# Optimization experiments

Measured on AMD Instinct MI355X. Metric: run time of the kernel, lower is better.

## Reference

```python
import jax, jax.numpy as jnp
import numpy as np

L = 8192
E = 1024
H = 16
D = E // H  # head_dim = 64


def setup_inputs() -> dict:
    key = jax.random.key(0)
    ks = jax.random.split(key, 5)
    x = jax.random.normal(ks[0], (L, E), dtype=jnp.float32)
    in_proj_weight = jax.random.normal(ks[1], (3 * E, E), dtype=jnp.float32) * (1.0 / np.sqrt(E))
    in_proj_bias = jax.random.normal(ks[2], (3 * E,), dtype=jnp.float32) * 0.02
    out_proj_weight = jax.random.normal(ks[3], (E, E), dtype=jnp.float32) * (1.0 / np.sqrt(E))
    out_proj_bias = jax.random.normal(ks[4], (E,), dtype=jnp.float32) * 0.02
    return {
        "x": x,
        "in_proj_weight": in_proj_weight,
        "in_proj_bias": in_proj_bias,
        "out_proj_weight": out_proj_weight,
        "out_proj_bias": out_proj_bias,
    }


def reference(x, in_proj_weight, in_proj_bias, out_proj_weight, out_proj_bias):
    # Single-token query (decode-style): q from x[:1], k/v from full sequence.
    q = x[:1] @ in_proj_weight[:E].T + in_proj_bias[:E]            # [1, E]
    k = x @ in_proj_weight[E:2 * E].T + in_proj_bias[E:2 * E]      # [L, E]
    v = x @ in_proj_weight[2 * E:].T + in_proj_bias[2 * E:]        # [L, E]

    q = q.reshape(1, H, D).transpose(1, 0, 2)   # [H, 1, D]
    k = k.reshape(L, H, D).transpose(1, 2, 0)   # [H, D, L]
    v = v.reshape(L, H, D).transpose(1, 0, 2)   # [H, L, D]

    scale = 1.0 / np.sqrt(D).astype(np.float32)
    dot = jnp.matmul(q, k) * scale              # [H, 1, L]
    attn = jax.nn.softmax(dot, axis=-1)
    out = jnp.matmul(attn, v)                   # [H, 1, D]
    out = out.transpose(1, 0, 2).reshape(1, E)  # [1, E]
    return out @ out_proj_weight.T + out_proj_bias
```

## Files before the change

kernel.cpp:

```cpp
#include <hip/hip_runtime.h>

#define LSEQ 8192
#define E 1024
#define H 16
#define NSHARD 16

typedef __attribute__((ext_vector_type(8))) short short8;
typedef __attribute__((ext_vector_type(4))) float f32x4;

__device__ inline float bf2f(unsigned int u16) {
    union { unsigned int i; float f; } v;
    v.i = (u16 & 0xffffu) << 16;
    return v.f;
}

__device__ inline unsigned short f2bf(float f) {
    union { float f; unsigned int i; } v; v.f = f;
    unsigned int x = v.i;
    return (unsigned short)((x + 0x7fffu + ((x >> 16) & 1u)) >> 16);
}

__device__ inline float wave_reduce_sum(float v) {
    #pragma unroll
    for (int off = 32; off > 0; off >>= 1) v += __shfl_xor(v, off, 64);
    return v;
}

__global__ __launch_bounds__(256) void k0_q(
    const float* __restrict__ x, const float* __restrict__ W,
    const float* __restrict__ bias, float* __restrict__ q_ws,
    float* __restrict__ S_shard)
{
    if (blockIdx.x == 0) S_shard[threadIdx.x] = 0.f;
    int wave = threadIdx.x >> 6, lane = threadIdx.x & 63;
    int i = blockIdx.x * 4 + wave;
    const f32x4* wp = (const f32x4*)(W + i * E) + lane * 4;
    const f32x4* xp = (const f32x4*)(x) + lane * 4;
    float s = 0.f;
    #pragma unroll
    for (int j = 0; j < 4; j++) {
        f32x4 w4 = wp[j], x4 = xp[j];
        s += w4[0]*x4[0] + w4[1]*x4[1] + w4[2]*x4[2] + w4[3]*x4[3];
    }
    s = wave_reduce_sum(s);
    if (lane == 0) q_ws[i] = s + bias[i];
}

__global__ __launch_bounds__(256) void k1_rc(
    const float* __restrict__ W, const float* __restrict__ bias,
    const float* __restrict__ q_ws, unsigned short* __restrict__ r_bf,
    float* __restrict__ c_ws)
{
    __shared__ float red[4][64];
    int hb = blockIdx.x >> 4, ec = blockIdx.x & 15;
    int lane = threadIdx.x & 63, wq = threadIdx.x >> 6;
    int e = ec * 64 + lane;
    const float* qh = q_ws + hb * 64;
    float acc = 0.f;
    #pragma unroll
    for (int i = 0; i < 16; i++) {
        int d = wq * 16 + i;
        acc += qh[d] * W[(E + hb * 64 + d) * E + e];
    }
    red[wq][lane] = acc;
    __syncthreads();
    if (wq == 0) {
        float s = red[0][lane] + red[1][lane] + red[2][lane] + red[3][lane];
        r_bf[hb * E + e] = f2bf(s * 0.125f);
    }
    if (ec == 0 && wq == 1) {
        float v = qh[lane] * bias[E + hb * 64 + lane];
        v = wave_reduce_sum(v);
        if (lane == 0) c_ws[hb] = v * 0.125f;
    }
}

__global__ __launch_bounds__(512, 1) void k2_fused(
    const float* __restrict__ x,
    const unsigned short* __restrict__ r_bf,
    const float* __restrict__ c_ws,
    unsigned int* __restrict__ partial_bf, float* __restrict__ S_shard)
{
    __shared__ float x_lds[16 * 1028];
    __shared__ float sp[8 * 64 * 4];
    __shared__ float p_lds[16 * 16];
    __shared__ float esum[16];

    const int tid  = threadIdx.x;
    const int wave = tid >> 6, lane = tid & 63;
    const int beta = blockIdx.x;

    if (tid < 16) esum[tid] = 0.f;
    float acc[32];
    #pragma unroll
    for (int i = 0; i < 32; i++) acc[i] = 0.f;
    int lbase = beta * 32;

    for (int t = 0; t < 2; t++) {
        int R0 = lbase + t * 16;
        __syncthreads();
        {
            int row = tid >> 5, ch = tid & 31;
            const f32x4* src = (const f32x4*)(x + (R0 + row) * E);
            float* dst = x_lds + row * 1028;
            #pragma unroll
            for (int j = 0; j < 8; j++) {
                int c4 = ch + 32 * j;
                *(f32x4*)(dst + c4 * 4) = src[c4];
            }
        }
        __syncthreads();
        {
            int rw = lane & 15, quad = lane >> 4;
            f32x4 sacc = {0.f, 0.f, 0.f, 0.f};
            const float* arow = x_lds + rw * 1028 + wave * 128 + quad * 8;
            const short8* bp = (const short8*)(r_bf + rw * E + wave * 128 + quad * 8);
            #pragma unroll
            for (int kk = 0; kk < 4; kk++) {
                f32x4 a0 = *(const f32x4*)(arow + kk * 32);
                f32x4 a1 = *(const f32x4*)(arow + kk * 32 + 4);
                short8 af;
                af[0] = (short)f2bf(a0[0]); af[1] = (short)f2bf(a0[1]);
                af[2] = (short)f2bf(a0[2]); af[3] = (short)f2bf(a0[3]);
                af[4] = (short)f2bf(a1[0]); af[5] = (short)f2bf(a1[1]);
                af[6] = (short)f2bf(a1[2]); af[7] = (short)f2bf(a1[3]);
                short8 bfr = bp[kk * 4];
                sacc = __builtin_amdgcn_mfma_f32_16x16x32_bf16(af, bfr, sacc, 0, 0, 0);
            }
            *(f32x4*)&sp[(wave * 64 + lane) * 4] = sacc;
        }
        __syncthreads();
        if (tid < 256) {
            int m = tid >> 4, hh = tid & 15;
            int ln = (m >> 2) * 16 + hh, rg = m & 3;
            float s = c_ws[hh];
            #pragma unroll
            for (int w = 0; w < 8; w++) s += sp[(w * 64 + ln) * 4 + rg];
            float p = __expf(s);
            p_lds[m * 16 + hh] = p;
            atomicAdd(&esum[hh], p);
        }
        __syncthreads();
        #pragma unroll 4
        for (int m = 0; m < 16; m++) {
            float2 xv = *(const float2*)&x_lds[m * 1028 + tid * 2];
            const f32x4* pp = (const f32x4*)&p_lds[m * 16];
            #pragma unroll
            for (int g = 0; g < 4; g++) {
                f32x4 pv = pp[g];
                acc[(g * 4 + 0) * 2 + 0] += pv[0] * xv.x;
                acc[(g * 4 + 0) * 2 + 1] += pv[0] * xv.y;
                acc[(g * 4 + 1) * 2 + 0] += pv[1] * xv.x;
                acc[(g * 4 + 1) * 2 + 1] += pv[1] * xv.y;
                acc[(g * 4 + 2) * 2 + 0] += pv[2] * xv.x;
                acc[(g * 4 + 2) * 2 + 1] += pv[2] * xv.y;
                acc[(g * 4 + 3) * 2 + 0] += pv[3] * xv.x;
                acc[(g * 4 + 3) * 2 + 1] += pv[3] * xv.y;
            }
        }
    }
    __syncthreads();
    #pragma unroll
    for (int h = 0; h < 16; h++) {
        unsigned int pk = (unsigned int)f2bf(acc[h * 2])
                        | ((unsigned int)f2bf(acc[h * 2 + 1]) << 16);
        partial_bf[(beta * 16 + h) * 512 + tid] = pk;
    }
    if (tid < 16) atomicAdd(&S_shard[(beta & 15) * 16 + tid], esum[tid]);
}

__global__ __launch_bounds__(512) void k3_reduce(
    const unsigned int* __restrict__ partial_bf, float2* __restrict__ u_ws2)
{
    __shared__ float red[8][64][2];
    int wave = threadIdx.x >> 6, lane = threadIdx.x & 63;
    int col = blockIdx.x * 64 + lane;
    float s0 = 0.f, s1 = 0.f;
    #pragma unroll 8
    for (int bb = wave; bb < 256; bb += 8) {
        unsigned int v = partial_bf[bb * 8192 + col];
        s0 += bf2f(v);
        s1 += bf2f(v >> 16);
    }
    red[wave][lane][0] = s0;
    red[wave][lane][1] = s1;
    __syncthreads();
    if (wave == 0) {
        float t0 = 0.f, t1 = 0.f;
        #pragma unroll
        for (int w = 0; w < 8; w++) { t0 += red[w][lane][0]; t1 += red[w][lane][1]; }
        float2 o; o.x = t0; o.y = t1;
        u_ws2[col] = o;
    }
}

__global__ __launch_bounds__(256) void k4_oh(
    const float* __restrict__ W, const float* __restrict__ bias,
    const float* __restrict__ u_ws, const float* __restrict__ S_shard,
    float* __restrict__ oh_ws)
{
    int wave = threadIdx.x >> 6, lane = threadIdx.x & 63;
    int i = blockIdx.x * 4 + wave;
    int h = i >> 6;
    float Sh = 0.f;
    #pragma unroll
    for (int sh = 0; sh < NSHARD; sh++) Sh += S_shard[sh * 16 + h];
    const f32x4* wp = (const f32x4*)(W + (2 * E + i) * E) + lane * 4;
    const f32x4* up = (const f32x4*)(u_ws + h * E) + lane * 4;
    float s = 0.f;
    #pragma unroll
    for (int j = 0; j < 4; j++) {
        f32x4 w4 = wp[j], u4 = up[j];
        s += w4[0]*u4[0] + w4[1]*u4[1] + w4[2]*u4[2] + w4[3]*u4[3];
    }
    s = wave_reduce_sum(s);
    if (lane == 0) oh_ws[i] = s / Sh + bias[2 * E + i];
}

__global__ __launch_bounds__(256) void k5_out(
    const float* __restrict__ Wout, const float* __restrict__ bout,
    const float* __restrict__ oh_ws, float* __restrict__ out)
{
    int wave = threadIdx.x >> 6, lane = threadIdx.x & 63;
    int j = blockIdx.x * 4 + wave;
    const f32x4* wp = (const f32x4*)(Wout + j * E) + lane * 4;
    const f32x4* op = (const f32x4*)(oh_ws) + lane * 4;
    float s = 0.f;
    #pragma unroll
    for (int jj = 0; jj < 4; jj++) {
        f32x4 w4 = wp[jj], o4 = op[jj];
        s += w4[0]*o4[0] + w4[1]*o4[1] + w4[2]*o4[2] + w4[3]*o4[3];
    }
    s = wave_reduce_sum(s);
    if (lane == 0) out[j] = s + bout[j];
}

extern "C" void kernel_launch(void* const* d_in, const int* in_sizes, int n_in,
                              void* d_out, int out_size, void* d_ws, size_t ws_size,
                              hipStream_t stream) {
    const float* x  = (const float*)d_in[0];
    const float* W  = (const float*)d_in[1];
    const float* b  = (const float*)d_in[2];
    const float* Wo = (const float*)d_in[3];
    const float* bo = (const float*)d_in[4];
    float* out = (float*)d_out;
    char* ws = (char*)d_ws;

    float* c_ws    = (float*)(ws);
    float* S_shard = (float*)(ws + 1024);
    float* oh_ws   = (float*)(ws + 4096);
    float* q_ws    = (float*)(ws + 12288);
    unsigned short* r_bf = (unsigned short*)(ws + 16384);
    float* u_ws    = (float*)(ws + 65536);
    unsigned int* partial_bf = (unsigned int*)(ws + 131072);

    hipLaunchKernelGGL(k0_q,     dim3(256), dim3(256), 0, stream,
                       x, W, b, q_ws, S_shard);
    hipLaunchKernelGGL(k1_rc,    dim3(256), dim3(256), 0, stream,
                       W, b, q_ws, r_bf, c_ws);
    hipLaunchKernelGGL(k2_fused, dim3(256), dim3(512), 0, stream,
                       x, r_bf, c_ws, partial_bf, S_shard);
    hipLaunchKernelGGL(k3_reduce, dim3(128), dim3(512), 0, stream,
                       partial_bf, (float2*)u_ws);
    hipLaunchKernelGGL(k4_oh,    dim3(256), dim3(256), 0, stream,
                       W, b, u_ws, S_shard, oh_ws);
    hipLaunchKernelGGL(k5_out,   dim3(256), dim3(256), 0, stream,
                       Wo, bo, oh_ws, out);
}
```

Before: 108.8 us.

## Halve k2 grid with 1024-thread blocks and register-prefetch next x tile

The fused score/accumulate kernel now runs 128 blocks of 1024 threads, each covering 64 sequence rows in four 16-row tiles instead of 256 blocks of 512 threads over 32 rows. The next tile of x is prefetched into registers while the current one is processed, to overlap global loads with compute. Each thread now owns one column instead of two and packs bf16 pairs via a lane shuffle. The reduction kernel reads half as many partials. The risk is that only 128 blocks leave half the CUs idle on a 256-CU part, and that per-block serial work goes up.

```diff
diff --git a/kernel.cpp b/kernel.cpp
--- a/kernel.cpp
+++ b/kernel.cpp
@@ -4,6 +4,7 @@
 #define E 1024
 #define H 16
 #define NSHARD 16
+#define NCHUNK 128
 
 typedef __attribute__((ext_vector_type(8))) short short8;
 typedef __attribute__((ext_vector_type(4))) float f32x4;
@@ -75,48 +76,56 @@
     }
 }
 
-__global__ __launch_bounds__(512, 1) void k2_fused(
+__global__ __launch_bounds__(1024, 1) void k2_fused(
     const float* __restrict__ x,
     const unsigned short* __restrict__ r_bf,
     const float* __restrict__ c_ws,
     unsigned int* __restrict__ partial_bf, float* __restrict__ S_shard)
 {
     __shared__ float x_lds[16 * 1028];
-    __shared__ float sp[8 * 64 * 4];
+    __shared__ float sp[16 * 64 * 4];
     __shared__ float p_lds[16 * 16];
     __shared__ float esum[16];
 
     const int tid  = threadIdx.x;
     const int wave = tid >> 6, lane = tid & 63;
     const int beta = blockIdx.x;
+    const int lbase = beta * 64;
 
     if (tid < 16) esum[tid] = 0.f;
-    float acc[32];
-    #pragma unroll
-    for (int i = 0; i < 32; i++) acc[i] = 0.f;
-    int lbase = beta * 32;
-
-    for (int t = 0; t < 2; t++) {
-        int R0 = lbase + t * 16;
+    float acc[16];
+    #pragma unroll
+    for (int i = 0; i < 16; i++) acc[i] = 0.f;
+
+    const int srow = tid >> 6, sch = tid & 63;
+    f32x4 pre[4];
+    {
+        const f32x4* src = (const f32x4*)(x + (lbase + srow) * E);
+        #pragma unroll
+        for (int j = 0; j < 4; j++) pre[j] = src[sch + 64 * j];
+    }
+
+    for (int t = 0; t < 4; t++) {
         __syncthreads();
         {
-            int row = tid >> 5, ch = tid & 31;
-            const f32x4* src = (const f32x4*)(x + (R0 + row) * E);
-            float* dst = x_lds + row * 1028;
-            #pragma unroll
-            for (int j = 0; j < 8; j++) {
-                int c4 = ch + 32 * j;
-                *(f32x4*)(dst + c4 * 4) = src[c4];
-            }
+            float* dst = x_lds + srow * 1028;
+            #pragma unroll
+            for (int j = 0; j < 4; j++) *(f32x4*)(dst + (sch + 64 * j) * 4) = pre[j];
+        }
+        {
+            int nt = (t + 1) & 3;
+            const f32x4* src = (const f32x4*)(x + (lbase + nt * 16 + srow) * E);
+            #pragma unroll
+            for (int j = 0; j < 4; j++) pre[j] = src[sch + 64 * j];
         }
         __syncthreads();
         {
             int rw = lane & 15, quad = lane >> 4;
             f32x4 sacc = {0.f, 0.f, 0.f, 0.f};
-            const float* arow = x_lds + rw * 1028 + wave * 128 + quad * 8;
-            const short8* bp = (const short8*)(r_bf + rw * E + wave * 128 + quad * 8);
-            #pragma unroll
-            for (int kk = 0; kk < 4; kk++) {
+            const float* arow = x_lds + rw * 1028 + wave * 64 + quad * 8;
+            const short8* bp = (const short8*)(r_bf + rw * E + wave * 64 + quad * 8);
+            #pragma unroll
+            for (int kk = 0; kk < 2; kk++) {
                 f32x4 a0 = *(const f32x4*)(arow + kk * 32);
                 f32x4 a1 = *(const f32x4*)(arow + kk * 32 + 4);
                 short8 af;
@@ -135,7 +144,7 @@
             int ln = (m >> 2) * 16 + hh, rg = m & 3;
             float s = c_ws[hh];
             #pragma unroll
-            for (int w = 0; w < 8; w++) s += sp[(w * 64 + ln) * 4 + rg];
+            for (int w = 0; w < 16; w++) s += sp[(w * 64 + ln) * 4 + rg];
             float p = __expf(s);
             p_lds[m * 16 + hh] = p;
             atomicAdd(&esum[hh], p);
@@ -143,30 +152,29 @@
         __syncthreads();
         #pragma unroll 4
         for (int m = 0; m < 16; m++) {
-            float2 xv = *(const float2*)&x_lds[m * 1028 + tid * 2];
+            float xv = x_lds[m * 1028 + tid];
             const f32x4* pp = (const f32x4*)&p_lds[m * 16];
             #pragma unroll
             for (int g = 0; g < 4; g++) {
                 f32x4 pv = pp[g];
-                acc[(g * 4 + 0) * 2 + 0] += pv[0] * xv.x;
-                acc[(g * 4 + 0) * 2 + 1] += pv[0] * xv.y;
-                acc[(g * 4 + 1) * 2 + 0] += pv[1] * xv.x;
-                acc[(g * 4 + 1) * 2 + 1] += pv[1] * xv.y;
-                acc[(g * 4 + 2) * 2 + 0] += pv[2] * xv.x;
-                acc[(g * 4 + 2) * 2 + 1] += pv[2] * xv.y;
-                acc[(g * 4 + 3) * 2 + 0] += pv[3] * xv.x;
-                acc[(g * 4 + 3) * 2 + 1] += pv[3] * xv.y;
+                acc[g * 4 + 0] += pv[0] * xv;
+                acc[g * 4 + 1] += pv[1] * xv;
+                acc[g * 4 + 2] += pv[2] * xv;
+                acc[g * 4 + 3] += pv[3] * xv;
             }
         }
     }
     __syncthreads();
-    #pragma unroll
-    for (int h = 0; h < 16; h++) {
-        unsigned int pk = (unsigned int)f2bf(acc[h * 2])
-                        | ((unsigned int)f2bf(acc[h * 2 + 1]) << 16);
-        partial_bf[(beta * 16 + h) * 512 + tid] = pk;
-    }
-    if (tid < 16) atomicAdd(&S_shard[(beta & 15) * 16 + tid], esum[tid]);
+    {
+        unsigned int* pb = partial_bf + beta * (H * 512);
+        #pragma unroll
+        for (int h = 0; h < 16; h++) {
+            unsigned int mine = (unsigned int)f2bf(acc[h]);
+            unsigned int other = (unsigned int)__shfl_xor((int)mine, 1, 64);
+            if ((tid & 1) == 0) pb[h * 512 + (tid >> 1)] = mine | (other << 16);
+        }
+        if (tid < 16) atomicAdd(&S_shard[(beta & 15) * 16 + tid], esum[tid]);
+    }
 }
 
 __global__ __launch_bounds__(512) void k3_reduce(
@@ -177,7 +185,7 @@
     int col = blockIdx.x * 64 + lane;
     float s0 = 0.f, s1 = 0.f;
     #pragma unroll 8
-    for (int bb = wave; bb < 256; bb += 8) {
+    for (int bb = wave; bb < NCHUNK; bb += 8) {
         unsigned int v = partial_bf[bb * 8192 + col];
         s0 += bf2f(v);
         s1 += bf2f(v >> 16);
@@ -258,7 +266,7 @@
                        x, W, b, q_ws, S_shard);
     hipLaunchKernelGGL(k1_rc,    dim3(256), dim3(256), 0, stream,
                        W, b, q_ws, r_bf, c_ws);
-    hipLaunchKernelGGL(k2_fused, dim3(256), dim3(512), 0, stream,
+    hipLaunchKernelGGL(k2_fused, dim3(128), dim3(1024), 0, stream,
                        x, r_bf, c_ws, partial_bf, S_shard);
     hipLaunchKernelGGL(k3_reduce, dim3(128), dim3(512), 0, stream,
                        partial_bf, (float2*)u_ws);
```

Measured after the change: 116.5 us. 1.07x slower.

## Load both 16-row tiles at once and widen reduce loads

Applied to the files above, without the earlier changes.

k2_fused now stages both 16-row x tiles into a doubled LDS buffer in one pass. Each half of the block's waves computes scores for one tile, with 4 waves covering K=256 each. This removes the two-iteration loop and its extra barriers and raises memory-level parallelism. LDS use roughly doubles to about 132KB, which limits the kernel to one block per CU (already implied by launch bounds). k3_reduce now reads uint2 per thread and writes float4, halving its grid, to make loads wider.

```diff
diff --git a/kernel.cpp b/kernel.cpp
--- a/kernel.cpp
+++ b/kernel.cpp
@@ -81,85 +81,89 @@
     const float* __restrict__ c_ws,
     unsigned int* __restrict__ partial_bf, float* __restrict__ S_shard)
 {
-    __shared__ float x_lds[16 * 1028];
-    __shared__ float sp[8 * 64 * 4];
-    __shared__ float p_lds[16 * 16];
+    __shared__ float x_lds[2 * 16 * 1028];
+    __shared__ float sp[2 * 4 * 64 * 4];
+    __shared__ float p_lds[2 * 256];
     __shared__ float esum[16];
 
     const int tid  = threadIdx.x;
     const int wave = tid >> 6, lane = tid & 63;
+    const int g = tid >> 8;
+    const int wq = wave & 3;
     const int beta = blockIdx.x;
+    const int R0 = beta * 32 + g * 16;
 
     if (tid < 16) esum[tid] = 0.f;
+
+    {
+        int gt = tid & 255;
+        int row = gt >> 4, ch = gt & 15;
+        const f32x4* src = (const f32x4*)(x + (R0 + row) * E);
+        f32x4* dst = (f32x4*)(x_lds + g * 16448 + row * 1028);
+        #pragma unroll
+        for (int j = 0; j < 16; j++) {
+            *(f32x4*)((float*)(x_lds + g * 16448 + row * 1028) + (ch + 16 * j) * 4)
+                = src[ch + 16 * j];
+        }
+        (void)dst;
+    }
+    __syncthreads();
+
+    {
+        int rw = lane & 15, quad = lane >> 4;
+        f32x4 sacc = {0.f, 0.f, 0.f, 0.f};
+        const float* arow = x_lds + g * 16448 + rw * 1028 + wq * 256 + quad * 8;
+        const short8* bp = (const short8*)(r_bf + rw * E + wq * 256 + quad * 8);
+        #pragma unroll
+        for (int kk = 0; kk < 8; kk++) {
+            f32x4 a0 = *(const f32x4*)(arow + kk * 32);
+            f32x4 a1 = *(const f32x4*)(arow + kk * 32 + 4);
+            short8 af;
+            af[0] = (short)f2bf(a0[0]); af[1] = (short)f2bf(a0[1]);
+            af[2] = (short)f2bf(a0[2]); af[3] = (short)f2bf(a0[3]);
+            af[4] = (short)f2bf(a1[0]); af[5] = (short)f2bf(a1[1]);
+            af[6] = (short)f2bf(a1[2]); af[7] = (short)f2bf(a1[3]);
+            short8 bfr = bp[kk * 4];
+            sacc = __builtin_amdgcn_mfma_f32_16x16x32_bf16(af, bfr, sacc, 0, 0, 0);
+        }
+        *(f32x4*)&sp[(wave * 64 + lane) * 4] = sacc;
+    }
+    __syncthreads();
+
+    {
+        int m = (tid >> 4) & 15, hh = tid & 15;
+        int ln = (m >> 2) * 16 + hh, rg = m & 3;
+        float s = c_ws[hh];
+        #pragma unroll
+        for (int w = 0; w < 4; w++) s += sp[((g * 4 + w) * 64 + ln) * 4 + rg];
+        float p = __expf(s);
+        p_lds[g * 256 + m * 16 + hh] = p;
+        atomicAdd(&esum[hh], p);
+    }
+    __syncthreads();
+
     float acc[32];
     #pragma unroll
     for (int i = 0; i < 32; i++) acc[i] = 0.f;
-    int lbase = beta * 32;
-
-    for (int t = 0; t < 2; t++) {
-        int R0 = lbase + t * 16;
-        __syncthreads();
-        {
-            int row = tid >> 5, ch = tid & 31;
-            const f32x4* src = (const f32x4*)(x + (R0 + row) * E);
-            float* dst = x_lds + row * 1028;
-            #pragma unroll
-            for (int j = 0; j < 8; j++) {
-                int c4 = ch + 32 * j;
-                *(f32x4*)(dst + c4 * 4) = src[c4];
-            }
-        }
-        __syncthreads();
-        {
-            int rw = lane & 15, quad = lane >> 4;
-            f32x4 sacc = {0.f, 0.f, 0.f, 0.f};
-            const float* arow = x_lds + rw * 1028 + wave * 128 + quad * 8;
-            const short8* bp = (const short8*)(r_bf + rw * E + wave * 128 + quad * 8);
-            #pragma unroll
-            for (int kk = 0; kk < 4; kk++) {
-                f32x4 a0 = *(const f32x4*)(arow + kk * 32);
-                f32x4 a1 = *(const f32x4*)(arow + kk * 32 + 4);
-                short8 af;
-                af[0] = (short)f2bf(a0[0]); af[1] = (short)f2bf(a0[1]);
-                af[2] = (short)f2bf(a0[2]); af[3] = (short)f2bf(a0[3]);
-                af[4] = (short)f2bf(a1[0]); af[5] = (short)f2bf(a1[1]);
-                af[6] = (short)f2bf(a1[2]); af[7] = (short)f2bf(a1[3]);
-                short8 bfr = bp[kk * 4];
-                sacc = __builtin_amdgcn_mfma_f32_16x16x32_bf16(af, bfr, sacc, 0, 0, 0);
-            }
-            *(f32x4*)&sp[(wave * 64 + lane) * 4] = sacc;
-        }
-        __syncthreads();
-        if (tid < 256) {
-            int m = tid >> 4, hh = tid & 15;
-            int ln = (m >> 2) * 16 + hh, rg = m & 3;
-            float s = c_ws[hh];
-            #pragma unroll
-            for (int w = 0; w < 8; w++) s += sp[(w * 64 + ln) * 4 + rg];
-            float p = __expf(s);
-            p_lds[m * 16 + hh] = p;
-            atomicAdd(&esum[hh], p);
-        }
-        __syncthreads();
-        #pragma unroll 4
-        for (int m = 0; m < 16; m++) {
-            float2 xv = *(const float2*)&x_lds[m * 1028 + tid * 2];
-            const f32x4* pp = (const f32x4*)&p_lds[m * 16];
-            #pragma unroll
-            for (int g = 0; g < 4; g++) {
-                f32x4 pv = pp[g];
-                acc[(g * 4 + 0) * 2 + 0] += pv[0] * xv.x;
-                acc[(g * 4 + 0) * 2 + 1] += pv[0] * xv.y;
-                acc[(g * 4 + 1) * 2 + 0] += pv[1] * xv.x;
-                acc[(g * 4 + 1) * 2 + 1] += pv[1] * xv.y;
-                acc[(g * 4 + 2) * 2 + 0] += pv[2] * xv.x;
-                acc[(g * 4 + 2) * 2 + 1] += pv[2] * xv.y;
-                acc[(g * 4 + 3) * 2 + 0] += pv[3] * xv.x;
-                acc[(g * 4 + 3) * 2 + 1] += pv[3] * xv.y;
-            }
-        }
-    }
-    __syncthreads();
+    #pragma unroll 4
+    for (int mi = 0; mi < 32; mi++) {
+        int gg = mi >> 4, mm = mi & 15;
+        float2 xv = *(const float2*)&x_lds[gg * 16448 + mm * 1028 + tid * 2];
+        const f32x4* pp = (const f32x4*)&p_lds[gg * 256 + mm * 16];
+        #pragma unroll
+        for (int gq = 0; gq < 4; gq++) {
+            f32x4 pv = pp[gq];
+            acc[(gq * 4 + 0) * 2 + 0] += pv[0] * xv.x;
+            acc[(gq * 4 + 0) * 2 + 1] += pv[0] * xv.y;
+            acc[(gq * 4 + 1) * 2 + 0] += pv[1] * xv.x;
+            acc[(gq * 4 + 1) * 2 + 1] += pv[1] * xv.y;
+            acc[(gq * 4 + 2) * 2 + 0] += pv[2] * xv.x;
+            acc[(gq * 4 + 2) * 2 + 1] += pv[2] * xv.y;
+            acc[(gq * 4 + 3) * 2 + 0] += pv[3] * xv.x;
+            acc[(gq * 4 + 3) * 2 + 1] += pv[3] * xv.y;
+        }
+    }
+
     #pragma unroll
     for (int h = 0; h < 16; h++) {
         unsigned int pk = (unsigned int)f2bf(acc[h * 2])
@@ -170,27 +174,29 @@
 }
 
 __global__ __launch_bounds__(512) void k3_reduce(
-    const unsigned int* __restrict__ partial_bf, float2* __restrict__ u_ws2)
-{
-    __shared__ float red[8][64][2];
-    int wave = threadIdx.x >> 6, lane = threadIdx.x & 63;
-    int col = blockIdx.x * 64 + lane;
-    float s0 = 0.f, s1 = 0.f;
+    const uint2* __restrict__ partial_u2, f32x4* __restrict__ u_ws4)
+{
+    __shared__ float red[8][64][4];
+    int wave = threadIdx.x >> 6, lane = threadIdx.x & 63;
+    int col2 = blockIdx.x * 64 + lane;
+    float s0 = 0.f, s1 = 0.f, s2 = 0.f, s3 = 0.f;
     #pragma unroll 8
     for (int bb = wave; bb < 256; bb += 8) {
-        unsigned int v = partial_bf[bb * 8192 + col];
-        s0 += bf2f(v);
-        s1 += bf2f(v >> 16);
-    }
-    red[wave][lane][0] = s0;
-    red[wave][lane][1] = s1;
+        uint2 v = partial_u2[bb * 4096 + col2];
+        s0 += bf2f(v.x); s1 += bf2f(v.x >> 16);
+        s2 += bf2f(v.y); s3 += bf2f(v.y >> 16);
+    }
+    red[wave][lane][0] = s0; red[wave][lane][1] = s1;
+    red[wave][lane][2] = s2; red[wave][lane][3] = s3;
     __syncthreads();
     if (wave == 0) {
-        float t0 = 0.f, t1 = 0.f;
-        #pragma unroll
-        for (int w = 0; w < 8; w++) { t0 += red[w][lane][0]; t1 += red[w][lane][1]; }
-        float2 o; o.x = t0; o.y = t1;
-        u_ws2[col] = o;
+        f32x4 t = {0.f, 0.f, 0.f, 0.f};
+        #pragma unroll
+        for (int w = 0; w < 8; w++) {
+            t[0] += red[w][lane][0]; t[1] += red[w][lane][1];
+            t[2] += red[w][lane][2]; t[3] += red[w][lane][3];
+        }
+        u_ws4[col2] = t;
     }
 }
 
@@ -260,8 +266,8 @@
                        W, b, q_ws, r_bf, c_ws);
     hipLaunchKernelGGL(k2_fused, dim3(256), dim3(512), 0, stream,
                        x, r_bf, c_ws, partial_bf, S_shard);
-    hipLaunchKernelGGL(k3_reduce, dim3(128), dim3(512), 0, stream,
-                       partial_bf, (float2*)u_ws);
+    hipLaunchKernelGGL(k3_reduce, dim3(64), dim3(512), 0, stream,
+                       (const uint2*)partial_bf, (f32x4*)u_ws);
     hipLaunchKernelGGL(k4_oh,    dim3(256), dim3(256), 0, stream,
                        W, b, u_ws, S_shard, oh_ws);
     hipLaunchKernelGGL(k5_out,   dim3(256), dim3(256), 0, stream,
```

Measured after the change: 108.4 us. About the same (-0.4%).
